# Optimization experiments

Hardware: AMD Instinct MI355X
Metric: run time of the kernel (lower is better)

## Reference

```python
import jax, jax.numpy as jnp
import numpy as np

N = 50000      # number of nodes (rows of edge_embeddings)
E = 800000     # number of edges
D = 256        # edge_dim
TOPK = 50


def setup_inputs() -> dict:
    key = jax.random.key(0)
    k1, k2, k3, k4, k5, k6 = jax.random.split(key, 6)
    edge_embeddings = jax.random.normal(k1, (N, D), dtype=jnp.float32)
    edge_index = jax.random.randint(k2, (2, E), 0, N, dtype=jnp.int64)
    # PyTorch nn.Linear default init: U(-1/sqrt(fan_in), 1/sqrt(fan_in))
    s1 = 1.0 / np.sqrt(2 * D)
    s2 = 1.0 / np.sqrt(D)
    W1 = jax.random.uniform(k3, (2 * D, D), jnp.float32, -s1, s1)
    b1 = jax.random.uniform(k4, (D,), jnp.float32, -s1, s1)
    W2 = jax.random.uniform(k5, (D, 1), jnp.float32, -s2, s2)
    b2 = jax.random.uniform(k6, (1,), jnp.float32, -s2, s2)
    return {"edge_embeddings": edge_embeddings, "W1": W1, "b1": b1,
            "W2": W2, "b2": b2, "edge_index": edge_index, "top_k": TOPK}


def reference(edge_embeddings, W1, b1, W2, b2, edge_index, top_k):
    src, dst = edge_index[0], edge_index[1]           # [E]
    valid = src < dst                                  # original keeps only i<j pairs
    # gather + concat: [E, 2D]
    pair_emb = jnp.concatenate([edge_embeddings[src], edge_embeddings[dst]], axis=-1)
    h = jax.nn.relu(pair_emb @ W1 + b1)                # [E, D]
    score = jax.nn.sigmoid(h @ W2 + b2)[:, 0]          # [E], in (0,1)
    # invalid edges get score -1 (< any sigmoid output) so topk picks only valid ones
    masked = jnp.where(valid, score, jnp.float32(-1.0))
    top_scores, top_idx = jax.lax.top_k(masked, top_k)
    top_pairs = edge_index[:, top_idx]                 # [2, k] (src,dst) of top edges
    return top_pairs, top_scores
```

## Files before the change

### kernel.cpp

```cpp
#include <hip/hip_runtime.h>
#include <hip/hip_bf16.h>
#include <cstdint>

#define TOPK 50
#define SUB_RANK 64
#define HIST_STRIDE 8
#define HIST_BINS 16384
#define CAND_CAP 16384
#define NFBLK 512
#define SORT_CAP 8192

typedef __attribute__((ext_vector_type(8))) short bf16x8;
typedef __attribute__((ext_vector_type(4))) float f32x4;

__device__ __forceinline__ unsigned short f2bf(float f) {
    unsigned u = __float_as_uint(f);
    u += 0x7FFFu + ((u >> 16) & 1u);
    return (unsigned short)(u >> 16);
}

__global__ __launch_bounds__(256) void prep_count(const float* __restrict__ W1,
                                                  unsigned* __restrict__ Wcf4,
                                                  unsigned* __restrict__ hist,
                                                  unsigned* __restrict__ misc,
                                                  const int* __restrict__ eidx,
                                                  unsigned* __restrict__ bcount, int E) {
    __shared__ int s_is64;
    if (threadIdx.x == 0) {
        int allz = 1;
        for (int q = 0; q < 64; ++q)
            if (eidx[2 * q + 1] != 0) { allz = 0; break; }
        s_is64 = allz;
    }
    __syncthreads();
    const int is64 = s_is64;

    int g = blockIdx.x * blockDim.x + threadIdx.x;
    if (g < 256 * 64) {
        int l = g & 63;
        int kt = (g >> 6) & 7;
        int nt = g >> 9;
        int col = nt * 16 + (l & 15);
        int kb = kt * 32 + (l >> 4) * 8;
        unsigned short h[8];
#pragma unroll
        for (int j = 0; j < 8; ++j) {
            int k = kb + j;
            float f = (col < 256) ? W1[k * 256 + col] : W1[(256 + k) * 256 + (col - 256)];
            h[j] = f2bf(f);
        }
        unsigned* dst = Wcf4 + (size_t)g * 4;
        dst[0] = (unsigned)h[0] | ((unsigned)h[1] << 16);
        dst[1] = (unsigned)h[2] | ((unsigned)h[3] << 16);
        dst[2] = (unsigned)h[4] | ((unsigned)h[5] << 16);
        dst[3] = (unsigned)h[6] | ((unsigned)h[7] << 16);
    }
    if (g < HIST_BINS) hist[g] = 0;
    if (g == 0) {
        misc[0] = (unsigned)is64;
        misc[2] = 0;
        misc[3] = 0;
        misc[4] = 0;
    }

    const int chunk = (E + gridDim.x - 1) / gridDim.x;
    const int lo = blockIdx.x * chunk;
    const int hi = min(E, lo + chunk);
    unsigned cnt = 0;
    for (int e = lo + threadIdx.x; e < hi; e += blockDim.x) {
        int s, d;
        if (is64) {
            s = ((const int2*)eidx)[e].x;
            d = ((const int2*)eidx)[(size_t)e + E].x;
        } else {
            s = eidx[e];
            d = eidx[e + E];
        }
        cnt += (s < d);
    }
#pragma unroll
    for (int off = 32; off; off >>= 1) cnt += __shfl_xor(cnt, off, 64);
    __shared__ unsigned wsum[4];
    if ((threadIdx.x & 63) == 0) wsum[threadIdx.x >> 6] = cnt;
    __syncthreads();
    if (threadIdx.x == 0)
        bcount[blockIdx.x] = wsum[0] + wsum[1] + wsum[2] + wsum[3];
}

__global__ __launch_bounds__(256) void gemm_plus_write(const float* __restrict__ emb,
                                                       const bf16x8* __restrict__ Bv,
                                                       const float* __restrict__ b1,
                                                       unsigned char* __restrict__ C8,
                                                       int M, int NG,
                                                       const int* __restrict__ eidx,
                                                       unsigned* __restrict__ misc,
                                                       const unsigned* __restrict__ bcount,
                                                       int* __restrict__ vsrc,
                                                       int* __restrict__ vdst,
                                                       int* __restrict__ vid, int E) {
    __shared__ uint4 afrag[2048];
    const int t = threadIdx.x;

    if ((int)blockIdx.x < NG) {
        const int w = t >> 6;
        const int l = t & 63;

        uint2* w2 = (uint2*)afrag;
#pragma unroll
        for (int iter = 0; iter < 16; ++iter) {
            int r = iter * 4 + w;
            int c0 = l * 4;
            int gr = blockIdx.x * 64 + r;
            float4 v = make_float4(0.f, 0.f, 0.f, 0.f);
            if (gr < M) v = *(const float4*)&emb[(size_t)gr * 256 + c0];
            unsigned u0 = (unsigned)f2bf(v.x) | ((unsigned)f2bf(v.y) << 16);
            unsigned u1 = (unsigned)f2bf(v.z) | ((unsigned)f2bf(v.w) << 16);
            int mt = r >> 4;
            int kt = c0 >> 5;
            int lane = (r & 15) + ((c0 & 31) >> 3) * 16;
            int f = mt * 8 + kt;
            int slot = f * 64 + (lane ^ (f & 7));
            w2[slot * 2 + ((c0 & 7) >> 2)] = make_uint2(u0, u1);
        }
        __syncthreads();

        const int wn = w;
#pragma unroll
        for (int nh = 0; nh < 2; ++nh) {
            f32x4 acc[4][4];
#pragma unroll
            for (int i = 0; i < 4; ++i)
#pragma unroll
                for (int j = 0; j < 4; ++j) acc[i][j] = (f32x4){0.f, 0.f, 0.f, 0.f};

            const int nt0 = wn * 8 + nh * 4;
            bf16x8 bcur[4];
#pragma unroll
            for (int j = 0; j < 4; ++j)
                bcur[j] = Bv[(size_t)((nt0 + j) * 8 + 0) * 64 + l];

#pragma unroll
            for (int kt = 0; kt < 8; ++kt) {
                bf16x8 af[4];
#pragma unroll
                for (int i = 0; i < 4; ++i)
                    af[i] = *(const bf16x8*)&afrag[(i * 8 + kt) * 64 + (l ^ kt)];
                bf16x8 bnxt[4];
                if (kt < 7) {
#pragma unroll
                    for (int j = 0; j < 4; ++j)
                        bnxt[j] = Bv[(size_t)((nt0 + j) * 8 + kt + 1) * 64 + l];
                }
#pragma unroll
                for (int i = 0; i < 4; ++i)
#pragma unroll
                    for (int j = 0; j < 4; ++j)
                        acc[i][j] = __builtin_amdgcn_mfma_f32_16x16x32_bf16(af[i], bcur[j], acc[i][j], 0, 0, 0);
                if (kt < 7) {
#pragma unroll
                    for (int j = 0; j < 4; ++j) bcur[j] = bnxt[j];
                }
            }

#pragma unroll
            for (int i = 0; i < 4; ++i) {
                int row0 = blockIdx.x * 64 + i * 16 + (l >> 4) * 4;
#pragma unroll
                for (int j = 0; j < 4; ++j) {
                    int col = (nt0 + j) * 16 + (l & 15);
                    float bias = (col < 256) ? b1[col] : 0.f;
#pragma unroll
                    for (int r = 0; r < 4; ++r) {
                        float v = acc[i][j][r] + bias;
                        int pk = __builtin_amdgcn_cvt_pk_fp8_f32(v, v, 0, false);
                        C8[(size_t)(row0 + r) * 512 + col] = (unsigned char)(pk & 0xFF);
                    }
                }
            }
        }
    } else {
        const int is64 = (int)misc[0];
        const int bid = (int)blockIdx.x - NG;
        unsigned* red = (unsigned*)afrag;
        unsigned* wcnt = red + 256;

        unsigned c0 = bcount[t], c1 = bcount[t + 256];
        unsigned pa = ((t < bid) ? c0 : 0u) + ((t + 256 < bid) ? c1 : 0u);
        red[t] = pa;
        __syncthreads();
        for (int s = 128; s; s >>= 1) {
            if (t < s) red[t] += red[t + s];
            __syncthreads();
        }
        const unsigned myoff = red[0];
        __syncthreads();
        red[t] = c0 + c1;
        __syncthreads();
        for (int s = 128; s; s >>= 1) {
            if (t < s) red[t] += red[t + s];
            __syncthreads();
        }
        if (bid == 0 && t == 0) misc[4] = red[0];

        const int chunk = (E + NFBLK - 1) / NFBLK;
        const int lo = bid * chunk;
        const int hi = min(E, lo + chunk);
        const int lane = t & 63;
        const int w = t >> 6;
        unsigned running = myoff;
        for (int base = lo; base < hi; base += blockDim.x) {
            int e = base + t;
            bool valid = false;
            int s = 0, d = 0;
            if (e < hi) {
                if (is64) {
                    s = ((const int2*)eidx)[e].x;
                    d = ((const int2*)eidx)[(size_t)e + E].x;
                } else {
                    s = eidx[e];
                    d = eidx[e + E];
                }
                valid = s < d;
            }
            unsigned long long m = __ballot(valid);
            unsigned pfx = __popcll(m & ((1ull << lane) - 1ull));
            if (lane == 0) wcnt[w] = __popcll(m);
            __syncthreads();
            unsigned wbase = running;
            for (int i = 0; i < w; ++i) wbase += wcnt[i];
            if (valid) {
                unsigned p = wbase + pfx;
                vsrc[p] = s;
                vdst[p] = d;
                vid[p] = e;
            }
            unsigned tot = wcnt[0] + wcnt[1] + wcnt[2] + wcnt[3];
            __syncthreads();
            running += tot;
        }
    }
}

__device__ __forceinline__ float dotq(unsigned a, unsigned b, float4 w) {
    float s;
    s  = fmaxf(__builtin_amdgcn_cvt_f32_fp8(a, 0) + __builtin_amdgcn_cvt_f32_fp8(b, 0), 0.f) * w.x;
    s += fmaxf(__builtin_amdgcn_cvt_f32_fp8(a, 1) + __builtin_amdgcn_cvt_f32_fp8(b, 1), 0.f) * w.y;
    s += fmaxf(__builtin_amdgcn_cvt_f32_fp8(a, 2) + __builtin_amdgcn_cvt_f32_fp8(b, 2), 0.f) * w.z;
    s += fmaxf(__builtin_amdgcn_cvt_f32_fp8(a, 3) + __builtin_amdgcn_cvt_f32_fp8(b, 3), 0.f) * w.w;
    return s;
}

__global__ __launch_bounds__(256) void edge_score_fp8(const unsigned char* __restrict__ C8,
                                                      const int* __restrict__ vsrc,
                                                      const int* __restrict__ vdst,
                                                      const float* __restrict__ W2,
                                                      const float* __restrict__ b2,
                                                      float* __restrict__ svals,
                                                      const unsigned* __restrict__ misc) {
    const int V = (int)misc[4];
    const int lane = threadIdx.x & 63;
    const int q = lane & 15;
    const int g = lane >> 4;
    const int wid = blockIdx.x * (blockDim.x >> 6) + (threadIdx.x >> 6);
    const int nw = gridDim.x * (blockDim.x >> 6);

    const float4 w0 = *(const float4*)&W2[q * 16 + 0];
    const float4 w1 = *(const float4*)&W2[q * 16 + 4];
    const float4 w2 = *(const float4*)&W2[q * 16 + 8];
    const float4 w3 = *(const float4*)&W2[q * 16 + 12];
    const float bb2 = b2[0];

    for (int base = wid * 4; base < V; base += nw * 4) {
        const int slot = base + g;
        const bool ok = slot < V;
        const int src = ok ? vsrc[slot] : 0;
        const int dst = ok ? vdst[slot] : 0;
        const uint4 ua = *(const uint4*)(C8 + (size_t)src * 512 + q * 16);
        const uint4 ub = *(const uint4*)(C8 + (size_t)dst * 512 + 256 + q * 16);
        float p = dotq(ua.x, ub.x, w0);
        p += dotq(ua.y, ub.y, w1);
        p += dotq(ua.z, ub.z, w2);
        p += dotq(ua.w, ub.w, w3);
        p += __shfl_xor(p, 1, 64);
        p += __shfl_xor(p, 2, 64);
        p += __shfl_xor(p, 4, 64);
        p += __shfl_xor(p, 8, 64);
        if (q == 0 && ok) {
            float z = p + bb2;
            float sc = 1.0f / (1.0f + expf(-z));
            svals[slot] = sc;
        }
    }
}

__global__ __launch_bounds__(256) void hist_kernel(const float* __restrict__ svals,
                                                   const unsigned* __restrict__ misc,
                                                   unsigned* __restrict__ hist) {
    __shared__ unsigned lh[HIST_BINS];
    const int V = (int)misc[4] / HIST_STRIDE;
    const int t = threadIdx.x;
    for (int i = t; i < HIST_BINS; i += 256) lh[i] = 0;
    __syncthreads();
    int i = blockIdx.x * blockDim.x + t;
    int stride = gridDim.x * blockDim.x;
    for (int v = i; v < V; v += stride)
        atomicAdd(&lh[__float_as_uint(svals[(size_t)v * HIST_STRIDE]) >> 16], 1u);
    __syncthreads();
    for (int b = t; b < HIST_BINS; b += 256) {
        unsigned c = lh[b];
        if (c) atomicAdd(&hist[b], c);
    }
}

__global__ __launch_bounds__(256) void compact(const float* __restrict__ svals,
                                               const int* __restrict__ vid,
                                               const unsigned* __restrict__ hist,
                                               unsigned* __restrict__ misc,
                                               unsigned long long* __restrict__ cand) {
    __shared__ unsigned chunk[256];
    __shared__ unsigned s_thr;
    const int t = threadIdx.x;
    {
        unsigned s = 0;
        for (int i = 0; i < 64; ++i) s += hist[t * 64 + i];
        chunk[t] = s;
    }
    __syncthreads();
    if (t == 0) {
        unsigned cum = 0;
        int c;
        unsigned thr = 0;
        for (c = 255; c >= 0; --c) {
            if (cum + chunk[c] >= SUB_RANK) break;
            cum += chunk[c];
        }
        if (c >= 0) {
            for (int b = c * 64 + 63; b >= c * 64; --b) {
                cum += hist[b];
                if (cum >= SUB_RANK) { thr = ((unsigned)b) << 16; break; }
            }
        }
        s_thr = thr;
    }
    __syncthreads();
    const unsigned thr = s_thr;

    const int V = (int)misc[4];
    int i = blockIdx.x * blockDim.x + t;
    int stride = gridDim.x * blockDim.x;
    for (int v = i; v < V; v += stride) {
        unsigned bits = __float_as_uint(svals[v]);
        if (bits >= thr) {
            unsigned pos = atomicAdd(&misc[3], 1u);
            if (pos < CAND_CAP)
                cand[pos] = ((unsigned long long)bits << 32) |
                            (unsigned)(0xFFFFFFFFu - (unsigned)vid[v]);
        }
    }
}

__global__ __launch_bounds__(256) void rescore(const float* __restrict__ emb,
                                               const float* __restrict__ W1,
                                               const float* __restrict__ b1,
                                               const float* __restrict__ W2,
                                               const float* __restrict__ b2,
                                               const int* __restrict__ eidx,
                                               const unsigned long long* __restrict__ cand,
                                               const unsigned* __restrict__ misc,
                                               unsigned long long* __restrict__ rescored,
                                               int E) {
    __shared__ float es[256], ed[256];
    __shared__ float red[256];
    const int C = (int)min(misc[3], (unsigned)CAND_CAP);
    const int is64 = (int)misc[0];
    const int t = threadIdx.x;
    for (int c = blockIdx.x; c < C; c += gridDim.x) {
        unsigned long long entry = cand[c];
        unsigned e = 0xFFFFFFFFu - (unsigned)(entry & 0xFFFFFFFFu);
        int src, dst;
        if (is64) {
            src = eidx[2 * (size_t)e];
            dst = eidx[2 * ((size_t)e + E)];
        } else {
            src = eidx[e];
            dst = eidx[e + E];
        }
        es[t] = emb[(size_t)src * 256 + t];
        ed[t] = emb[(size_t)dst * 256 + t];
        __syncthreads();
        float h = b1[t];
#pragma unroll 8
        for (int k = 0; k < 256; ++k) h += es[k] * W1[k * 256 + t];
#pragma unroll 8
        for (int k = 0; k < 256; ++k) h += ed[k] * W1[(256 + k) * 256 + t];
        red[t] = fmaxf(h, 0.f) * W2[t];
        __syncthreads();
        for (int s = 128; s; s >>= 1) {
            if (t < s) red[t] += red[t + s];
            __syncthreads();
        }
        if (t == 0) {
            float z = red[0] + b2[0];
            float sc = 1.0f / (1.0f + expf(-z));
            rescored[c] = ((unsigned long long)__float_as_uint(sc) << 32) |
                          (unsigned)(0xFFFFFFFFu - e);
        }
        __syncthreads();
    }
}

__global__ __launch_bounds__(256) void final_topk(unsigned long long* __restrict__ rescored,
                                                  const unsigned* __restrict__ misc,
                                                  const int* __restrict__ eidx,
                                                  float* __restrict__ out, int E) {
    __shared__ unsigned long long a[SORT_CAP];
    const int t = threadIdx.x;
    const int C = (int)min(misc[3], (unsigned)CAND_CAP);
    const int is64 = (int)misc[0];

    if (C <= SORT_CAP) {
        int n = 256;
        while (n < C) n <<= 1;
        for (int i = t; i < n; i += 256) a[i] = (i < C) ? rescored[i] : 0ull;
        __syncthreads();
        for (int k = 2; k <= n; k <<= 1) {
            for (int j = k >> 1; j > 0; j >>= 1) {
                for (int i = t; i < n; i += 256) {
                    int ixj = i ^ j;
                    if (ixj > i) {
                        unsigned long long x = a[i], y = a[ixj];
                        bool sw = ((i & k) == 0) ? (x < y) : (x > y);
                        if (sw) { a[i] = y; a[ixj] = x; }
                    }
                }
                __syncthreads();
            }
        }
        if (t < TOPK) {
            unsigned long long m = a[t];
            if (m != 0ull) {
                unsigned bits = (unsigned)(m >> 32);
                unsigned e = 0xFFFFFFFFu - (unsigned)(m & 0xFFFFFFFFu);
                int src, dst;
                if (is64) {
                    src = eidx[2 * (size_t)e];
                    dst = eidx[2 * ((size_t)e + E)];
                } else {
                    src = eidx[e];
                    dst = eidx[e + E];
                }
                out[t] = (float)src;
                out[TOPK + t] = (float)dst;
                out[2 * TOPK + t] = __uint_as_float(bits);
            } else {
                out[t] = -1.f;
                out[TOPK + t] = -1.f;
                out[2 * TOPK + t] = -1.f;
            }
        }
        return;
    }

    __shared__ unsigned long long red[256];
    for (int r = 0; r < TOPK; ++r) {
        unsigned long long best = 0ull;
        for (int i = t; i < C; i += 256) {
            unsigned long long v = rescored[i];
            if (v > best) best = v;
        }
        red[t] = best;
        __syncthreads();
        for (int s = 128; s; s >>= 1) {
            if (t < s) {
                if (red[t + s] > red[t]) red[t] = red[t + s];
            }
            __syncthreads();
        }
        unsigned long long m = red[0];
        __syncthreads();
        for (int i = t; i < C; i += 256)
            if (rescored[i] == m) rescored[i] = 0ull;
        if (t == 0) {
            if (m != 0ull) {
                unsigned bits = (unsigned)(m >> 32);
                unsigned e = 0xFFFFFFFFu - (unsigned)(m & 0xFFFFFFFFu);
                int src, dst;
                if (is64) {
                    src = eidx[2 * (size_t)e];
                    dst = eidx[2 * ((size_t)e + E)];
                } else {
                    src = eidx[e];
                    dst = eidx[e + E];
                }
                out[r] = (float)src;
                out[TOPK + r] = (float)dst;
                out[2 * TOPK + r] = __uint_as_float(bits);
            } else {
                out[r] = -1.f;
                out[TOPK + r] = -1.f;
                out[2 * TOPK + r] = -1.f;
            }
        }
        __syncthreads();
    }
}

extern "C" void kernel_launch(void* const* d_in, const int* in_sizes, int n_in,
                              void* d_out, int out_size, void* d_ws, size_t ws_size,
                              hipStream_t stream) {
    const float* emb = (const float*)d_in[0];
    const float* W1  = (const float*)d_in[1];
    const float* b1  = (const float*)d_in[2];
    const float* W2  = (const float*)d_in[3];
    const float* b2  = (const float*)d_in[4];
    const int*   eidx = (const int*)d_in[5];

    const int M = in_sizes[0] / 256;
    const int E = in_sizes[5] / 2;
    const int Mpad = ((M + 63) / 64) * 64;
    const int NG = Mpad / 64;

    char* p = (char*)d_ws;
    auto alloc = [&](size_t bytes) {
        char* r = p;
        p += (bytes + 255) & ~(size_t)255;
        return r;
    };
    unsigned* Wcf4 = (unsigned*)alloc(256 * 512 * 2);
    unsigned char* C8 = (unsigned char*)alloc((size_t)Mpad * 512);
    float* svals = (float*)alloc((size_t)E * 4);
    int* vsrc = (int*)alloc((size_t)E * 4);
    int* vdst = (int*)alloc((size_t)E * 4);
    int* vid  = (int*)alloc((size_t)E * 4);
    unsigned* hist = (unsigned*)alloc(HIST_BINS * 4);
    unsigned long long* cand = (unsigned long long*)alloc(CAND_CAP * 8);
    unsigned long long* resc = (unsigned long long*)alloc(CAND_CAP * 8);
    unsigned* bcount = (unsigned*)alloc(NFBLK * 4);
    unsigned* misc = (unsigned*)alloc(256);

    float* out = (float*)d_out;

    prep_count<<<NFBLK, 256, 0, stream>>>(W1, Wcf4, hist, misc, eidx, bcount, E);

    gemm_plus_write<<<NG + NFBLK, 256, 0, stream>>>(emb, (const bf16x8*)Wcf4, b1, C8,
                                                    M, NG, eidx, misc, bcount,
                                                    vsrc, vdst, vid, E);

    edge_score_fp8<<<2048, 256, 0, stream>>>(C8, vsrc, vdst, W2, b2, svals, misc);

    hist_kernel<<<128, 256, 0, stream>>>(svals, misc, hist);

    compact<<<512, 256, 0, stream>>>(svals, vid, hist, misc, cand);

    rescore<<<1024, 256, 0, stream>>>(emb, W1, b1, W2, b2, eidx, cand, misc, resc, E);

    final_topk<<<1, 256, 0, stream>>>(resc, misc, eidx, out, E);
}
```

Baseline: 142.4 us.

## Move valid-edge counting into compaction blocks with atomic offset allocation

The edge-validity count moves out of the prep kernel and into each compaction block of the fused GEMM kernel. Each block now claims its output base with an atomicAdd instead of prefix-summing per-block counts, and the prep kernel shrinks to 64 blocks. This removes a full pass over edge_index from the prep stage and the per-block reduction barriers. In exchange, compacted edges land in nondeterministic block order and each compaction block reads its edge range twice.

New measurement: 156.0 us. +9.6%, slower.

```diff
diff --git a/kernel.cpp b/kernel.cpp
--- a/kernel.cpp
+++ b/kernel.cpp
@@ -19,24 +19,13 @@
     return (unsigned short)(u >> 16);
 }
 
-__global__ __launch_bounds__(256) void prep_count(const float* __restrict__ W1,
+__global__ __launch_bounds__(256) void prep_small(const float* __restrict__ W1,
                                                   unsigned* __restrict__ Wcf4,
                                                   unsigned* __restrict__ hist,
                                                   unsigned* __restrict__ misc,
-                                                  const int* __restrict__ eidx,
-                                                  unsigned* __restrict__ bcount, int E) {
-    __shared__ int s_is64;
-    if (threadIdx.x == 0) {
-        int allz = 1;
-        for (int q = 0; q < 64; ++q)
-            if (eidx[2 * q + 1] != 0) { allz = 0; break; }
-        s_is64 = allz;
-    }
-    __syncthreads();
-    const int is64 = s_is64;
-
+                                                  const int* __restrict__ eidx) {
     int g = blockIdx.x * blockDim.x + threadIdx.x;
-    if (g < 256 * 64) {
+    {
         int l = g & 63;
         int kt = (g >> 6) & 7;
         int nt = g >> 9;
@@ -57,34 +46,13 @@
     }
     if (g < HIST_BINS) hist[g] = 0;
     if (g == 0) {
-        misc[0] = (unsigned)is64;
-        misc[2] = 0;
+        int allz = 1;
+        for (int q = 0; q < 64; ++q)
+            if (eidx[2 * q + 1] != 0) { allz = 0; break; }
+        misc[0] = (unsigned)allz;
         misc[3] = 0;
         misc[4] = 0;
     }
-
-    const int chunk = (E + gridDim.x - 1) / gridDim.x;
-    const int lo = blockIdx.x * chunk;
-    const int hi = min(E, lo + chunk);
-    unsigned cnt = 0;
-    for (int e = lo + threadIdx.x; e < hi; e += blockDim.x) {
-        int s, d;
-        if (is64) {
-            s = ((const int2*)eidx)[e].x;
-            d = ((const int2*)eidx)[(size_t)e + E].x;
-        } else {
-            s = eidx[e];
-            d = eidx[e + E];
-        }
-        cnt += (s < d);
-    }
-#pragma unroll
-    for (int off = 32; off; off >>= 1) cnt += __shfl_xor(cnt, off, 64);
-    __shared__ unsigned wsum[4];
-    if ((threadIdx.x & 63) == 0) wsum[threadIdx.x >> 6] = cnt;
-    __syncthreads();
-    if (threadIdx.x == 0)
-        bcount[blockIdx.x] = wsum[0] + wsum[1] + wsum[2] + wsum[3];
 }
 
 __global__ __launch_bounds__(256) void gemm_plus_write(const float* __restrict__ emb,
@@ -94,7 +62,6 @@
                                                        int M, int NG,
                                                        const int* __restrict__ eidx,
                                                        unsigned* __restrict__ misc,
-                                                       const unsigned* __restrict__ bcount,
                                                        int* __restrict__ vsrc,
                                                        int* __restrict__ vdst,
                                                        int* __restrict__ vid, int E) {
@@ -183,31 +150,36 @@
         const int bid = (int)blockIdx.x - NG;
         unsigned* red = (unsigned*)afrag;
         unsigned* wcnt = red + 256;
-
-        unsigned c0 = bcount[t], c1 = bcount[t + 256];
-        unsigned pa = ((t < bid) ? c0 : 0u) + ((t + 256 < bid) ? c1 : 0u);
-        red[t] = pa;
-        __syncthreads();
-        for (int s = 128; s; s >>= 1) {
-            if (t < s) red[t] += red[t + s];
-            __syncthreads();
-        }
-        const unsigned myoff = red[0];
-        __syncthreads();
-        red[t] = c0 + c1;
-        __syncthreads();
-        for (int s = 128; s; s >>= 1) {
-            if (t < s) red[t] += red[t + s];
-            __syncthreads();
-        }
-        if (bid == 0 && t == 0) misc[4] = red[0];
+        unsigned* sbase = wcnt + 4;
 
         const int chunk = (E + NFBLK - 1) / NFBLK;
         const int lo = bid * chunk;
         const int hi = min(E, lo + chunk);
         const int lane = t & 63;
         const int w = t >> 6;
-        unsigned running = myoff;
+
+        unsigned cnt = 0;
+        for (int e = lo + t; e < hi; e += blockDim.x) {
+            int s, d;
+            if (is64) {
+                s = ((const int2*)eidx)[e].x;
+                d = ((const int2*)eidx)[(size_t)e + E].x;
+            } else {
+                s = eidx[e];
+                d = eidx[e + E];
+            }
+            cnt += (s < d);
+        }
+#pragma unroll
+        for (int off = 32; off; off >>= 1) cnt += __shfl_xor(cnt, off, 64);
+        if (lane == 0) wcnt[w] = cnt;
+        __syncthreads();
+        if (t == 0)
+            sbase[0] = atomicAdd(&misc[4], wcnt[0] + wcnt[1] + wcnt[2] + wcnt[3]);
+        __syncthreads();
+        unsigned running = sbase[0];
+        __syncthreads();
+
         for (int base = lo; base < hi; base += blockDim.x) {
             int e = base + t;
             bool valid = false;
@@ -535,15 +507,14 @@
     unsigned* hist = (unsigned*)alloc(HIST_BINS * 4);
     unsigned long long* cand = (unsigned long long*)alloc(CAND_CAP * 8);
     unsigned long long* resc = (unsigned long long*)alloc(CAND_CAP * 8);
-    unsigned* bcount = (unsigned*)alloc(NFBLK * 4);
     unsigned* misc = (unsigned*)alloc(256);
 
     float* out = (float*)d_out;
 
-    prep_count<<<NFBLK, 256, 0, stream>>>(W1, Wcf4, hist, misc, eidx, bcount, E);
+    prep_small<<<64, 256, 0, stream>>>(W1, Wcf4, hist, misc, eidx);
 
     gemm_plus_write<<<NG + NFBLK, 256, 0, stream>>>(emb, (const bf16x8*)Wcf4, b1, C8,
-                                                    M, NG, eidx, misc, bcount,
+                                                    M, NG, eidx, misc,
                                                     vsrc, vdst, vid, E);
 
     edge_score_fp8<<<2048, 256, 0, stream>>>(C8, vsrc, vdst, W2, b2, svals, misc);
```
